# Performance work log

Hardware: AMD Instinct MI355X
Metric: run time of the kernel (lower is better)

Reference implementation:

```python
import jax, jax.numpy as jnp
import numpy as np

B, C, N = 4, 512, 4096
CH = C // 2  # query/key projection dim


def setup_inputs() -> dict:
    key = jax.random.key(0)
    ks = jax.random.split(key, 10)
    s = 1.0 / np.sqrt(C)
    return {
        "Q": jax.random.normal(ks[0], (B, C, N), dtype=jnp.float32),
        "K": jax.random.normal(ks[1], (B, C, N), dtype=jnp.float32),
        "V": jax.random.normal(ks[2], (B, C, N), dtype=jnp.float32),
        "Wq": jax.random.normal(ks[3], (CH, C), dtype=jnp.float32) * s,
        "bq": jax.random.normal(ks[4], (CH,), dtype=jnp.float32) * s,
        "Wk": jax.random.normal(ks[5], (CH, C), dtype=jnp.float32) * s,
        "bk": jax.random.normal(ks[6], (CH,), dtype=jnp.float32) * s,
        "Wv": jax.random.normal(ks[7], (C, C), dtype=jnp.float32) * s,
        "bv": jax.random.normal(ks[8], (C,), dtype=jnp.float32) * s,
        "gamma": jnp.full((1,), 0.5, dtype=jnp.float32),  # torch inits to 0; nonzero for meaningful math
    }


def reference(Q, K, V, Wq, bq, Wk, bk, Wv, bv, gamma):
    # Conv1d(kernel_size=1) == per-position linear over channels
    q = jnp.einsum("oc,bcn->bon", Wq, Q) + bq[None, :, None]  # [B, C/2, N]
    k = jnp.einsum("oc,bcn->bon", Wk, K) + bk[None, :, None]  # [B, C/2, N]
    v = jnp.einsum("oc,bcn->bon", Wv, V) + bv[None, :, None]  # [B, C, N]
    # energy[b,n,m] = <q[b,:,n], k[b,:,m]>  (no 1/sqrt(d) scaling in original)
    energy = jnp.einsum("bcn,bcm->bnm", q, k)                 # [B, N, N]
    attention = jax.nn.softmax(energy, axis=-1)
    # out[b,c,n] = sum_m v[b,c,m] * attention[b,n,m]
    out = jnp.einsum("bcm,bnm->bcn", v, attention)            # [B, C, N]
    return gamma * out + V
```

## Files before the change

kernel.cpp:

```cpp
#include <hip/hip_runtime.h>
#include <cstdint>
#include <cstddef>

constexpr int B_  = 4;
constexpr int C_  = 512;
constexpr int CH_ = 256;
constexpr int N_  = 4096;
#define LOG2E 1.4426950408889634f

typedef float    f32x4 __attribute__((ext_vector_type(4)));
typedef _Float16 f16x8 __attribute__((ext_vector_type(8)));
typedef _Float16 f16x4 __attribute__((ext_vector_type(4)));

__device__ __forceinline__ f32x4 MFMA16(f16x8 a, f16x8 b, f32x4 c) {
  return __builtin_amdgcn_mfma_f32_16x16x32_f16(a, b, c, 0, 0, 0);
}

typedef const __attribute__((address_space(1))) unsigned int* gas_u32p;
typedef __attribute__((address_space(3))) unsigned int* las_u32p;
__device__ __forceinline__ void async16(const void* g, void* l) {
  __builtin_amdgcn_global_load_lds((gas_u32p)g, (las_u32p)l, 16, 0, 0);
}

template <int CTRL>
__device__ __forceinline__ float dppmax(float x) {
  float y = __builtin_bit_cast(
      float, __builtin_amdgcn_update_dpp(0, __builtin_bit_cast(int, x), CTRL,
                                         0xF, 0xF, true));
  return fmaxf(x, y);
}
__device__ __forceinline__ float rowmax16(float x) {
  x = dppmax<0x128>(x); x = dppmax<0x124>(x);
  x = dppmax<0x122>(x); x = dppmax<0x121>(x);
  return x;
}

__global__ void prep_w_kernel(const float* __restrict__ Wq,
                              const float* __restrict__ Wk,
                              const float* __restrict__ Wv,
                              _Float16* __restrict__ wq,
                              _Float16* __restrict__ wk,
                              _Float16* __restrict__ wv) {
  int i = blockIdx.x * 256 + threadIdx.x;
  if (i < CH_ * C_) {
    wq[i] = (_Float16)(Wq[i] * LOG2E);
    wk[i] = (_Float16)Wk[i];
  }
  if (i < C_ * C_) wv[i] = (_Float16)Wv[i];
}

__global__ __launch_bounds__(512, 4) void proj_kernel(
    const _Float16* __restrict__ wq, const _Float16* __restrict__ wk,
    const _Float16* __restrict__ wv, const float* __restrict__ Q,
    const float* __restrict__ K, const float* __restrict__ V,
    const float* __restrict__ bq, const float* __restrict__ bk,
    const float* __restrict__ bv, _Float16* __restrict__ qT,
    _Float16* __restrict__ kT, _Float16* __restrict__ vT) {
  __shared__ __align__(16) _Float16 lW[2][256 * 32];

  const int y = blockIdx.y;
  const _Float16* W;
  const float* X;
  const float* bias;
  _Float16* out;
  int o0 = 0, M, mode;
  float bscale = 1.0f;
  if (y == 0) {
    W = wq; X = Q; bias = bq; out = qT; M = CH_; mode = 0; bscale = LOG2E;
  } else if (y == 1) {
    W = wk; X = K; bias = bk; out = kT; M = CH_; mode = 0;
  } else {
    W = wv; X = V; bias = bv; out = vT; M = C_; mode = 1; o0 = (y - 2) * 256;
  }

  const int tid = threadIdx.x;
  const int lane = tid & 63, wave = tid >> 6;
  const int g = lane >> 4, lm = lane & 15;
  const int b = blockIdx.z;
  const int n0 = blockIdx.x * 64;
  const int wo = (wave >> 1) * 64, wn = (wave & 1) * 32;

  const _Float16* Wb = W + (size_t)o0 * C_;
  const float* Xb = X + (size_t)b * C_ * N_;
  const int ncol = n0 + wn + lm;

  f32x4 acc[8];
#pragma unroll
  for (int i = 0; i < 8; ++i) acc[i] = f32x4{0.f, 0.f, 0.f, 0.f};

  auto stageW = [&](int s, int buf) {
    int c0 = s * 32;
#pragma unroll
    for (int r = 0; r < 2; ++r) {
      int ci = r * 512 + tid;
      int o = ci >> 2, cg = ci & 3;
      async16(Wb + (size_t)o * C_ + c0 + cg * 8,
              (char*)&lW[buf][0] + r * 8192 + wave * 1024);
    }
  };

  float xr[2][2][8];
  auto loadX = [&](int s, int buf) {
    int c0 = s * 32;
#pragma unroll
    for (int nt = 0; nt < 2; ++nt) {
      const float* xp = Xb + (size_t)(c0 + g * 8) * N_ + ncol + nt * 16;
#pragma unroll
      for (int j = 0; j < 8; ++j) xr[buf][nt][j] = xp[(size_t)j * N_];
    }
  };

  stageW(0, 0);
  loadX(0, 0);

#pragma unroll
  for (int s = 0; s < 16; ++s) {
    __syncthreads();
    if (s < 15) {
      stageW(s + 1, (s + 1) & 1);
      loadX(s + 1, (s + 1) & 1);
    }
    f16x8 xf[2];
#pragma unroll
    for (int nt = 0; nt < 2; ++nt)
#pragma unroll
      for (int j = 0; j < 8; ++j) xf[nt][j] = (_Float16)xr[s & 1][nt][j];
    const _Float16* pw = &lW[s & 1][0];
    f16x8 wf[4];
#pragma unroll
    for (int ot = 0; ot < 4; ++ot)
      wf[ot] = *(const f16x8*)(pw + ((wo + ot * 16 + lm) * 4 + g) * 8);
    if (mode == 0) {
#pragma unroll
      for (int nt = 0; nt < 2; ++nt)
#pragma unroll
        for (int ot = 0; ot < 4; ++ot)
          acc[nt * 4 + ot] = MFMA16(xf[nt], wf[ot], acc[nt * 4 + ot]);
    } else {
#pragma unroll
      for (int ot = 0; ot < 4; ++ot)
#pragma unroll
        for (int nt = 0; nt < 2; ++nt)
          acc[ot * 2 + nt] = MFMA16(wf[ot], xf[nt], acc[ot * 2 + nt]);
    }
  }

  if (mode == 0) {
#pragma unroll
    for (int nt = 0; nt < 2; ++nt) {
#pragma unroll
      for (int ot = 0; ot < 4; ++ot) {
        int o = wo + ot * 16 + lm;
        float bv_ = bias[o] * bscale;
#pragma unroll
        for (int r = 0; r < 4; ++r) {
          int n = n0 + wn + nt * 16 + g * 4 + r;
          out[((size_t)b * N_ + n) * M + o] =
              (_Float16)(acc[nt * 4 + ot][r] + bv_);
        }
      }
    }
  } else {
#pragma unroll
    for (int ot = 0; ot < 4; ++ot) {
#pragma unroll
      for (int r = 0; r < 4; ++r) {
        int o = o0 + wo + ot * 16 + g * 4 + r;
        float bv_ = bias[o];
#pragma unroll
        for (int nt = 0; nt < 2; ++nt) {
          int n = n0 + wn + nt * 16 + lm;
          out[((size_t)b * M + o) * N_ + n] =
              (_Float16)(acc[ot * 2 + nt][r] + bv_);
        }
      }
    }
  }
}

__global__ __launch_bounds__(512, 2) void attn_kernel(
    const _Float16* __restrict__ qT, const _Float16* __restrict__ kT,
    const _Float16* __restrict__ vT, float* __restrict__ Op0,
    _Float16* __restrict__ Op1, float* __restrict__ mbuf,
    float* __restrict__ lbuf) {
  __shared__ __align__(16) _Float16 kstage[2 * 8192];
  __shared__ __align__(16) _Float16 P_t[128 * 72];
  __shared__ float al_st[128];
  __shared__ int bumped[8];

  const int tid = threadIdx.x;
  const int lane = tid & 63, wave = tid >> 6;
  const int g = lane >> 4, lm = lane & 15;

  const int bx = blockIdx.x;
  const int xcd = bx & 7;
  const int b = xcd >> 1, h = xcd & 1;
  const int n0 = (bx >> 3) * 128;
  const int mbase = h * 2048;
  const int c0w = wave * 64;

  f32x4 O[4][8];
#pragma unroll
  for (int i = 0; i < 4; ++i)
#pragma unroll
    for (int j = 0; j < 8; ++j) O[i][j] = f32x4{0.f, 0.f, 0.f, 0.f};
  f32x4 Ol = f32x4{0.f, 0.f, 0.f, 0.f};

  const _Float16* qTb = qT + ((size_t)b * N_ + n0) * CH_;
  f16x8 qf[8];
#pragma unroll
  for (int p = 0; p < 2; ++p) {
#pragma unroll
    for (int r = 0; r < 4; ++r) {
      int sidx = r * 512 + tid;
      int rl = sidx >> 5, cgs = sidx & 31;
      async16(qTb + (size_t)(p * 64 + rl) * CH_ + ((cgs ^ (rl & 7)) * 8),
              (char*)kstage + r * 8192 + wave * 1024);
    }
    __syncthreads();
    if ((wave >> 2) == p) {
      int rl = (wave & 3) * 16 + lm;
#pragma unroll
      for (int ks = 0; ks < 8; ++ks)
        qf[ks] =
            *(const f16x8*)&kstage[rl * 256 + (((ks * 4 + g) ^ (rl & 7)) * 8)];
    }
    __syncthreads();
  }

  const _Float16* kTb = kT + ((size_t)b * N_ + mbase) * CH_;
  auto stage_k = [&](int it) {
    int m0 = it * 32;
    char* dst0 = (char*)kstage + (it & 1) * 16384;
#pragma unroll
    for (int r = 0; r < 2; ++r) {
      int sidx = r * 512 + tid;
      int key = sidx >> 5, cgs = sidx & 31;
      async16(kTb + (size_t)(m0 + key) * CH_ + ((cgs ^ (key & 7)) * 8),
              dst0 + r * 8192 + wave * 1024);
    }
  };
  stage_k(0);

  const _Float16* vTb = vT + (size_t)b * C_ * N_ + mbase;
  const _Float16* vbase[4];
#pragma unroll
  for (int ct = 0; ct < 4; ++ct)
    vbase[ct] = vTb + (size_t)(c0w + ct * 16 + lm) * N_ + g * 8;
  f16x8 vf[4], vfn[4];
#pragma unroll
  for (int ct = 0; ct < 4; ++ct) vf[ct] = *(const f16x8*)vbase[ct];

  f32x4 m_run = f32x4{-1e30f, -1e30f, -1e30f, -1e30f};
  f16x8 ones;
#pragma unroll
  for (int i = 0; i < 8; ++i) ones[i] = (_Float16)1.0f;

#pragma unroll 1
  for (int it = 0; it < 64; ++it) {
    __syncthreads();
    if (it < 63) stage_k(it + 1);

    const _Float16* kb = kstage + (it & 1) * 8192;
    f32x4 s0 = f32x4{0.f, 0.f, 0.f, 0.f};
    f32x4 s1 = f32x4{0.f, 0.f, 0.f, 0.f};
    const int key0 = lm, key1 = 16 + lm;
#pragma unroll
    for (int ks = 0; ks < 8; ++ks) {
      f16x8 kf0 =
          *(const f16x8*)&kb[key0 * 256 + (((ks * 4 + g) ^ (key0 & 7)) * 8)];
      f16x8 kf1 =
          *(const f16x8*)&kb[key1 * 256 + (((ks * 4 + g) ^ (key1 & 7)) * 8)];
      s0 = MFMA16(qf[ks], kf0, s0);
      s1 = MFMA16(qf[ks], kf1, s1);
    }

    f32x4 alpha;
    bool anyb = false;
#pragma unroll
    for (int r = 0; r < 4; ++r) {
      float mx = rowmax16(fmaxf(s0[r], s1[r]));
      float mnew = fmaxf(m_run[r], mx);
      alpha[r] = exp2f(m_run[r] - mnew);
      anyb |= (mnew > m_run[r]);
      m_run[r] = mnew;
      float p0 = exp2f(s0[r] - mnew);
      float p1 = exp2f(s1[r] - mnew);
      int row = wave * 16 + g * 4 + r;
      P_t[row * 72 + lm] = (_Float16)p0;
      P_t[row * 72 + 16 + lm] = (_Float16)p1;
    }
    if (lm == 0) *(f32x4*)&al_st[wave * 16 + g * 4] = alpha;
    unsigned long long bal = __ballot(anyb);
    if (lane == 0) bumped[wave] = (bal != 0ull) ? 1 : 0;
    __syncthreads();

    if (it < 63) {
      int mo = (it + 1) * 32;
#pragma unroll
      for (int ct = 0; ct < 4; ++ct)
        vfn[ct] = *(const f16x8*)(vbase[ct] + mo);
    }

#pragma unroll
    for (int nt = 0; nt < 8; ++nt) {
      if (__builtin_amdgcn_readfirstlane(bumped[nt])) {
        float a = al_st[nt * 16 + lm];
#pragma unroll
        for (int ct = 0; ct < 4; ++ct) {
          O[ct][nt][0] *= a; O[ct][nt][1] *= a;
          O[ct][nt][2] *= a; O[ct][nt][3] *= a;
        }
      }
    }
    if (__builtin_amdgcn_readfirstlane(bumped[wave])) {
      float a = al_st[wave * 16 + lm];
      Ol[0] *= a; Ol[1] *= a; Ol[2] *= a; Ol[3] *= a;
    }

#pragma unroll
    for (int nt = 0; nt < 8; ++nt) {
      f16x8 pf = *(const f16x8*)&P_t[(nt * 16 + lm) * 72 + g * 8];
#pragma unroll
      for (int ct = 0; ct < 4; ++ct) O[ct][nt] = MFMA16(vf[ct], pf, O[ct][nt]);
    }
    {
      f16x8 pfo = *(const f16x8*)&P_t[(wave * 16 + lm) * 72 + g * 8];
      Ol = MFMA16(ones, pfo, Ol);
    }
    if (it < 63) {
#pragma unroll
      for (int ct = 0; ct < 4; ++ct) vf[ct] = vfn[ct];
    }
  }

  const size_t hb = (size_t)(b * 2 + h) * N_ + n0;
  if (lm == 0) {
#pragma unroll
    for (int r = 0; r < 4; ++r) mbuf[hb + wave * 16 + g * 4 + r] = m_run[r];
  }
  if (lane < 16) lbuf[hb + wave * 16 + lane] = Ol[0];

  if (h == 0) {
    float* ob = Op0 + (size_t)b * C_ * N_;
#pragma unroll
    for (int nt = 0; nt < 8; ++nt) {
      int n_g = n0 + nt * 16 + lm;
#pragma unroll
      for (int ct = 0; ct < 4; ++ct) {
        int cb = c0w + ct * 16 + g * 4;
#pragma unroll
        for (int r = 0; r < 4; ++r)
          ob[(size_t)(cb + r) * N_ + n_g] = O[ct][nt][r];
      }
    }
  } else {
    _Float16* ob = Op1 + (size_t)b * C_ * N_;
#pragma unroll
    for (int nt = 0; nt < 8; ++nt) {
      int n_g = n0 + nt * 16 + lm;
#pragma unroll
      for (int ct = 0; ct < 4; ++ct) {
        int cb = c0w + ct * 16 + g * 4;
#pragma unroll
        for (int r = 0; r < 4; ++r)
          ob[(size_t)(cb + r) * N_ + n_g] = (_Float16)O[ct][nt][r];
      }
    }
  }
}

__global__ __launch_bounds__(256) void combine_kernel(
    float* __restrict__ out, const _Float16* __restrict__ Op1,
    const float* __restrict__ mbuf, const float* __restrict__ lbuf,
    const float* __restrict__ Vin, const float* __restrict__ gptr) {
  const int b = blockIdx.y;
  const int tid = threadIdx.x;
  const int n = blockIdx.x * 64 + (tid & 15) * 4;
  const int cg = tid >> 4;
  const float gamma = gptr[0];

  float s0[4], s1[4];
#pragma unroll
  for (int j = 0; j < 4; ++j) {
    float m0 = mbuf[(size_t)(b * 2 + 0) * N_ + n + j];
    float m1 = mbuf[(size_t)(b * 2 + 1) * N_ + n + j];
    float mx = fmaxf(m0, m1);
    float a0 = exp2f(m0 - mx), a1 = exp2f(m1 - mx);
    float l = a0 * lbuf[(size_t)(b * 2 + 0) * N_ + n + j] +
              a1 * lbuf[(size_t)(b * 2 + 1) * N_ + n + j];
    float inv = gamma / l;
    s0[j] = a0 * inv;
    s1[j] = a1 * inv;
  }

  const _Float16* O1b = Op1 + (size_t)b * C_ * N_;
  for (int c = cg * 32; c < cg * 32 + 32; ++c) {
    size_t idx = ((size_t)b * C_ + c) * N_ + n;
    f32x4 p0 = *(const f32x4*)(out + idx);
    f16x4 p1 = *(const f16x4*)(O1b + (size_t)c * N_ + n);
    f32x4 V = *(const f32x4*)(Vin + idx);
    f32x4 r;
#pragma unroll
    for (int j = 0; j < 4; ++j)
      r[j] = p0[j] * s0[j] + (float)p1[j] * s1[j] + V[j];
    *(f32x4*)(out + idx) = r;
  }
}

extern "C" void kernel_launch(void* const* d_in, const int* in_sizes, int n_in,
                              void* d_out, int out_size, void* d_ws, size_t ws_size,
                              hipStream_t stream) {
  const float* Q  = (const float*)d_in[0];
  const float* K  = (const float*)d_in[1];
  const float* V  = (const float*)d_in[2];
  const float* Wq = (const float*)d_in[3];
  const float* bq = (const float*)d_in[4];
  const float* Wk = (const float*)d_in[5];
  const float* bk = (const float*)d_in[6];
  const float* Wv = (const float*)d_in[7];
  const float* bv = (const float*)d_in[8];
  const float* gm = (const float*)d_in[9];
  float* out = (float*)d_out;

  char* p = (char*)d_ws;
  _Float16* wq = (_Float16*)p; p += (size_t)CH_ * C_ * 2;
  _Float16* wk = (_Float16*)p; p += (size_t)CH_ * C_ * 2;
  _Float16* wv = (_Float16*)p; p += (size_t)C_ * C_ * 2;
  _Float16* qT = (_Float16*)p; p += (size_t)B_ * N_ * CH_ * 2;
  _Float16* kT = (_Float16*)p; p += (size_t)B_ * N_ * CH_ * 2;
  _Float16* vT = (_Float16*)p; p += (size_t)B_ * C_ * N_ * 2;
  _Float16* Op1 = (_Float16*)p; p += (size_t)B_ * C_ * N_ * 2;
  float* mbuf = (float*)p; p += (size_t)B_ * 2 * N_ * 4;
  float* lbuf = (float*)p; p += (size_t)B_ * 2 * N_ * 4;

  prep_w_kernel<<<(C_ * C_) / 256, 256, 0, stream>>>(Wq, Wk, Wv, wq, wk, wv);

  proj_kernel<<<dim3(N_ / 64, 4, B_), 512, 0, stream>>>(
      wq, wk, wv, Q, K, V, bq, bk, bv, qT, kT, vT);

  attn_kernel<<<256, 512, 0, stream>>>(qT, kT, vT, out, Op1, mbuf, lbuf);

  combine_kernel<<<dim3(N_ / 64, B_), 256, 0, stream>>>(out, Op1, mbuf, lbuf,
                                                        V, gm);
}
```

Before: 400.0 us.

## Stage projection input X through swizzled LDS with coalesced vector loads

The projection kernel now reads X with coalesced 16-byte row loads, one float4 per thread per stage, instead of strided per-lane scalar column loads. It converts the values to fp16 and writes them into a double-buffered, XOR-swizzled LDS tile, from which the MFMA operands are read as f16x8. The global loads are prefetched two stages ahead and the barrier moves to the end of each iteration. This adds LDS traffic and an extra LDS buffer, which may lower occupancy, in exchange for better global-load coalescing.

```diff
diff --git a/kernel.cpp b/kernel.cpp
--- a/kernel.cpp
+++ b/kernel.cpp
@@ -57,6 +57,7 @@
     const float* __restrict__ bv, _Float16* __restrict__ qT,
     _Float16* __restrict__ kT, _Float16* __restrict__ vT) {
   __shared__ __align__(16) _Float16 lW[2][256 * 32];
+  __shared__ __align__(16) _Float16 lX[2][64 * 56];
 
   const int y = blockIdx.y;
   const _Float16* W;
@@ -82,7 +83,6 @@
 
   const _Float16* Wb = W + (size_t)o0 * C_;
   const float* Xb = X + (size_t)b * C_ * N_;
-  const int ncol = n0 + wn + lm;
 
   f32x4 acc[8];
 #pragma unroll
@@ -99,37 +99,45 @@
     }
   };
 
-  float xr[2][2][8];
-  auto loadX = [&](int s, int buf) {
-    int c0 = s * 32;
+  const int xc = tid >> 4;
+  const int xn4 = (tid & 15) * 4;
+  const int xgran = xc >> 3, xcin = xc & 7;
+  auto gloadX = [&](int s) {
+    return *(const f32x4*)(Xb + (size_t)(s * 32 + xc) * N_ + n0 + xn4);
+  };
+  auto writeX = [&](int buf, f32x4 v) {
+#pragma unroll
+    for (int i = 0; i < 4; ++i) {
+      int n = xn4 + i;
+      int pos = (xgran ^ ((n >> 2) & 3)) * 8 + xcin;
+      lX[buf][n * 56 + pos] = (_Float16)v[i];
+    }
+  };
+
+  f32x4 xg = gloadX(0);
+  writeX(0, xg);
+  xg = gloadX(1);
+  stageW(0, 0);
+  __syncthreads();
+
+#pragma unroll
+  for (int s = 0; s < 16; ++s) {
+    const int cb = s & 1, nb = cb ^ 1;
+    if (s < 15) stageW(s + 1, nb);
+    f32x4 xgn;
+    if (s < 14) xgn = gloadX(s + 2);
+
+    f16x8 wf[4], xf[2];
+#pragma unroll
+    for (int ot = 0; ot < 4; ++ot)
+      wf[ot] = *(const f16x8*)&lW[cb][((wo + ot * 16 + lm) * 4 + g) * 8];
 #pragma unroll
     for (int nt = 0; nt < 2; ++nt) {
-      const float* xp = Xb + (size_t)(c0 + g * 8) * N_ + ncol + nt * 16;
-#pragma unroll
-      for (int j = 0; j < 8; ++j) xr[buf][nt][j] = xp[(size_t)j * N_];
-    }
-  };
-
-  stageW(0, 0);
-  loadX(0, 0);
-
-#pragma unroll
-  for (int s = 0; s < 16; ++s) {
-    __syncthreads();
-    if (s < 15) {
-      stageW(s + 1, (s + 1) & 1);
-      loadX(s + 1, (s + 1) & 1);
-    }
-    f16x8 xf[2];
-#pragma unroll
-    for (int nt = 0; nt < 2; ++nt)
-#pragma unroll
-      for (int j = 0; j < 8; ++j) xf[nt][j] = (_Float16)xr[s & 1][nt][j];
-    const _Float16* pw = &lW[s & 1][0];
-    f16x8 wf[4];
-#pragma unroll
-    for (int ot = 0; ot < 4; ++ot)
-      wf[ot] = *(const f16x8*)(pw + ((wo + ot * 16 + lm) * 4 + g) * 8);
+      int n = wn + nt * 16 + lm;
+      int pos = (g ^ ((n >> 2) & 3)) * 8;
+      xf[nt] = *(const f16x8*)&lX[cb][n * 56 + pos];
+    }
+
     if (mode == 0) {
 #pragma unroll
       for (int nt = 0; nt < 2; ++nt)
@@ -143,6 +151,10 @@
         for (int nt = 0; nt < 2; ++nt)
           acc[ot * 2 + nt] = MFMA16(wf[ot], xf[nt], acc[ot * 2 + nt]);
     }
+
+    if (s < 15) writeX(nb, xg);
+    if (s < 14) xg = xgn;
+    __syncthreads();
   }
 
   if (mode == 0) {
```

New measurement: 376.7 us. -5.8%, faster.
